# Kernel tuning notes

Measured on AMD Instinct MI355X. Metric: run time of the kernel, lower is better.

The kernel has to match this reference:

```python
import jax, jax.numpy as jnp
import numpy as np

B, S, H = 2, 2048, 2048
NH, NKV, HD = 32, 8, 64
G = NH // NKV  # query heads per KV head
SCALE = HD ** -0.5
NEG = -1e9


def setup_inputs() -> dict:
    key = jax.random.key(0)
    ks = jax.random.split(key, 6)
    hidden_states = jax.random.normal(ks[0], (B, S, H), dtype=jnp.float32)
    # causal additive mask, broadcastable over batch and heads
    causal = jnp.tril(jnp.ones((S, S), dtype=bool))
    attention_mask = jnp.where(causal, 0.0, NEG).astype(jnp.float32)[None, None]
    sd = 1.0 / np.sqrt(H)
    wq = jax.random.normal(ks[1], (H, NH * HD), dtype=jnp.float32) * sd
    wk = jax.random.normal(ks[2], (H, NKV * HD), dtype=jnp.float32) * sd
    wv = jax.random.normal(ks[3], (H, NKV * HD), dtype=jnp.float32) * sd
    wo = jax.random.normal(ks[4], (NH * HD, H), dtype=jnp.float32) * sd
    return {"hidden_states": hidden_states, "attention_mask": attention_mask,
            "wq": wq, "wk": wk, "wv": wv, "wo": wo}


def reference(hidden_states, attention_mask, wq, wk, wv, wo):
    b, s, _ = hidden_states.shape
    # projections; group q heads as [b, kv_head, group, s, d] to avoid
    # materializing expanded K/V (same math as expand+matmul)
    q = (hidden_states @ wq).reshape(b, s, NKV, G, HD)
    k = (hidden_states @ wk).reshape(b, s, NKV, HD)
    v = (hidden_states @ wv).reshape(b, s, NKV, HD)
    q = jnp.einsum('bskgd->bkgsd', q)
    k = jnp.einsum('bskd->bksd', k)
    v = jnp.einsum('bskd->bksd', v)
    scores = jnp.einsum('bkgsd,bktd->bkgst', q, k) * SCALE  # [b,kv,G,s,s]
    mask = attention_mask  # [1,1,S,S] broadcastable
    scores = scores + mask[:, :, None] if mask.ndim == 4 else scores + mask
    attn = jax.nn.softmax(scores.astype(jnp.float32), axis=-1).astype(q.dtype)
    out = jnp.einsum('bkgst,bktd->bkgsd', attn, v)
    out = jnp.einsum('bkgsd->bskgd', out).reshape(b, s, NH * HD)
    return out @ wo
```

## Files before the change

### kernel.cpp

```cpp
#include <hip/hip_runtime.h>
#include <hip/hip_bf16.h>
#include <type_traits>


#define B_SZ 2
#define S_LEN 2048
#define HID 2048
#define NHEADS 32
#define NKVH 8
#define HEADD 64
#define QKV_N 3072
#define QK_SCALE 0.18033688f

typedef __attribute__((ext_vector_type(8))) short bf16x8;
typedef __attribute__((ext_vector_type(4))) float f32x4;

__device__ __forceinline__ float bf2f(unsigned short u) {
  union { unsigned int i; float f; } v;
  v.i = ((unsigned int)u) << 16;
  return v.f;
}
__device__ __forceinline__ unsigned short f2bf(float f) {
  union { float f; unsigned int i; } v;
  v.f = f;
  unsigned int r = v.i + 0x7fffu + ((v.i >> 16) & 1u);
  return (unsigned short)(r >> 16);
}
__device__ __forceinline__ unsigned short f2bf_rn(float f) {
  union { __hip_bfloat16 h; unsigned short u; } cv;
  cv.h = __float2bfloat16(f);
  return cv.u;
}
#if __has_builtin(__builtin_amdgcn_exp2f)
__device__ __forceinline__ float exp2v(float x) { return __builtin_amdgcn_exp2f(x); }
#else
__device__ __forceinline__ float exp2v(float x) { return exp2f(x); }
#endif
__device__ __forceinline__ void gload_lds16(const unsigned short* g, unsigned short* l) {
  __builtin_amdgcn_global_load_lds(
      (const __attribute__((address_space(1))) unsigned int*)g,
      (__attribute__((address_space(3))) unsigned int*)l, 16, 0, 0);
}

__global__ void cvt_bf16_kernel(const float4* __restrict__ in,
                                ushort4* __restrict__ out, int n4) {
  int i = blockIdx.x * blockDim.x + threadIdx.x;
  if (i >= n4) return;
  float4 v = in[i];
  ushort4 o;
  o.x = f2bf(v.x); o.y = f2bf(v.y); o.z = f2bf(v.z); o.w = f2bf(v.w);
  out[i] = o;
}

__global__ void transpose_cvt_kernel(const float* __restrict__ in,
                                     unsigned short* __restrict__ out,
                                     int R, int C, float scale) {
  __shared__ float tile[32][33];
  int c0 = blockIdx.x * 32, r0 = blockIdx.y * 32;
  int x = threadIdx.x, y = threadIdx.y;
#pragma unroll
  for (int i = 0; i < 32; i += 8)
    tile[y + i][x] = in[(size_t)(r0 + y + i) * C + c0 + x];
  __syncthreads();
#pragma unroll
  for (int i = 0; i < 32; i += 8)
    out[(size_t)(c0 + y + i) * R + r0 + x] = f2bf(tile[x][y + i] * scale);
}

__global__ void transpose_v_kernel(const unsigned short* __restrict__ QKV,
                                   unsigned short* __restrict__ Vt) {
  __shared__ unsigned short tile[32][33];
  int s0 = blockIdx.x * 32, d0 = blockIdx.y * 32;
  int bk = blockIdx.z;
  int b = bk >> 3, kvh = bk & 7;
  int x = threadIdx.x, y = threadIdx.y;
#pragma unroll
  for (int i = 0; i < 32; i += 8)
    tile[y + i][x] =
        QKV[(size_t)(b * S_LEN + s0 + y + i) * QKV_N + 2560 + kvh * HEADD + d0 + x];
  __syncthreads();
#pragma unroll
  for (int i = 0; i < 32; i += 8)
    Vt[((size_t)(b * NKVH + kvh) * HEADD + d0 + y + i) * S_LEN + s0 + x] =
        tile[x][y + i];
}

template <typename OutT>
__global__ __launch_bounds__(256) void gemm_bt_kernel(
    const unsigned short* __restrict__ A, const unsigned short* __restrict__ Bt,
    OutT* __restrict__ C, int M, int N, int K) {
  __shared__ unsigned short ldsA[2][128 * 32];
  __shared__ unsigned short ldsB[2][128 * 32];
  const int tid = threadIdx.x;
  const int wave = tid >> 6;
  const int lane = tid & 63;
  const int nwg = gridDim.x;
  const int orig = blockIdx.x;
  const int swz = (orig & 7) * (nwg >> 3) + (orig >> 3);
  const int ntn = N >> 7;
  const int m0 = (swz / ntn) << 7;
  const int n0 = (swz % ntn) << 7;
  const int wr = wave >> 1, wc = wave & 1;
  f32x4 acc[4][4] = {};

  size_t offA[2], offB[2];
#pragma unroll
  for (int i = 0; i < 2; ++i) {
    int cc = tid + i * 256;
    int row = cc >> 2, slot = cc & 3;
    int xk = (slot ^ (row & 3)) * 8;
    offA[i] = (size_t)(m0 + row) * K + xk;
    offB[i] = (size_t)(n0 + row) * K + xk;
  }
  const int rl = lane & 15, g = lane >> 4;
  const int nk = K >> 5;

#pragma unroll
  for (int i = 0; i < 2; ++i) {
    gload_lds16(A + offA[i], &ldsA[0][(wave * 64 + i * 256) * 8]);
    gload_lds16(Bt + offB[i], &ldsB[0][(wave * 64 + i * 256) * 8]);
  }
  __syncthreads();
  int cur = 0;

  for (int t = 0; t < nk; ++t) {
    if (t + 1 < nk) {
      const int k0 = (t + 1) << 5;
      const int nb = cur ^ 1;
#pragma unroll
      for (int i = 0; i < 2; ++i) {
        gload_lds16(A + offA[i] + k0, &ldsA[nb][(wave * 64 + i * 256) * 8]);
        gload_lds16(Bt + offB[i] + k0, &ldsB[nb][(wave * 64 + i * 256) * 8]);
      }
    }
    const int xs = (g ^ (rl & 3)) * 8;
    bf16x8 a[4], b[4];
#pragma unroll
    for (int mi = 0; mi < 4; ++mi)
      a[mi] = *(const bf16x8*)&ldsA[cur][(wr * 64 + mi * 16 + rl) * 32 + xs];
#pragma unroll
    for (int ni = 0; ni < 4; ++ni)
      b[ni] = *(const bf16x8*)&ldsB[cur][(wc * 64 + ni * 16 + rl) * 32 + xs];
#pragma unroll
    for (int mi = 0; mi < 4; ++mi)
#pragma unroll
      for (int ni = 0; ni < 4; ++ni)
        acc[mi][ni] =
            __builtin_amdgcn_mfma_f32_16x16x32_bf16(a[mi], b[ni], acc[mi][ni], 0, 0, 0);
    __syncthreads();
    cur ^= 1;
  }
#pragma unroll
  for (int mi = 0; mi < 4; ++mi)
#pragma unroll
    for (int ni = 0; ni < 4; ++ni)
#pragma unroll
      for (int r = 0; r < 4; ++r) {
        int row = m0 + wr * 64 + mi * 16 + (lane >> 4) * 4 + r;
        int col = n0 + wc * 64 + ni * 16 + (lane & 15);
        float v = acc[mi][ni][r];
        if constexpr (std::is_same_v<OutT, unsigned short>)
          C[(size_t)row * N + col] = f2bf(v);
        else
          C[(size_t)row * N + col] = v;
      }
}

__global__ __launch_bounds__(256) void mfma_attn_kernel(
    const unsigned short* __restrict__ QKV,
    const unsigned short* __restrict__ Vt,
    unsigned short* __restrict__ O) {
  __shared__ unsigned short Ks[2][64 * 64];
  __shared__ unsigned short Vs[2][64 * 64];
  __shared__ unsigned short Pl[4 * 16 * 64];
  const int head = blockIdx.y, b = blockIdx.z;
  const int kvh = head >> 2;
  const int tid = threadIdx.x;
  const int w = tid >> 6, lane = tid & 63;
  const int c = lane & 15, g = lane >> 4;
  unsigned short* Plw = Pl + w * 1024;
  const int srow = tid >> 3, sslot = tid & 7;
  const int xslot = sslot ^ (srow & 7);

  const unsigned short* Ksrc[2];
  const unsigned short* Vsrc[2];
#pragma unroll
  for (int i = 0; i < 2; ++i) {
    int row = srow + i * 32;
    Ksrc[i] = QKV + (size_t)(b * S_LEN + row) * QKV_N + 2048 + kvh * HEADD + xslot * 8;
    Vsrc[i] = Vt + ((size_t)(b * NKVH + kvh) * HEADD + row) * S_LEN + xslot * 8;
  }

#pragma unroll
  for (int i = 0; i < 2; ++i) {
    gload_lds16(Ksrc[i], &Ks[0][(w * 64 + i * 256) * 8]);
    gload_lds16(Vsrc[i], &Vs[0][(w * 64 + i * 256) * 8]);
  }
  __syncthreads();
  int cur = 0;

  for (int ph = 0; ph < 2; ++ph) {
    const int qt = (ph == 0) ? (int)blockIdx.x : (S_LEN / 64 - 1) - (int)blockIdx.x;
    bf16x8 qf[2];
    {
      const unsigned short* qp =
          QKV + (size_t)(b * S_LEN + qt * 64 + w * 16 + c) * QKV_N + head * HEADD +
          g * 8;
      qf[0] = *(const bf16x8*)(qp);
      qf[1] = *(const bf16x8*)(qp + 32);
    }
    f32x4 o_acc[4] = {};
    float mstate = -INFINITY;
    float lstate = 0.f;

    for (int t = 0; t <= qt; ++t) {
      const int kv0 = t * 64;
      const bool has_next = !(ph == 1 && t == qt);
      if (has_next) {
        const int kvn = (t < qt) ? kv0 + 64 : 0;
        const int nb = cur ^ 1;
#pragma unroll
        for (int i = 0; i < 2; ++i) {
          gload_lds16(Ksrc[i] + (size_t)kvn * QKV_N, &Ks[nb][(w * 64 + i * 256) * 8]);
          gload_lds16(Vsrc[i] + kvn, &Vs[nb][(w * 64 + i * 256) * 8]);
        }
      }
      f32x4 s_acc[4] = {};
      __builtin_amdgcn_s_setprio(1);
#pragma unroll
      for (int ks = 0; ks < 2; ++ks)
#pragma unroll
        for (int kn = 0; kn < 4; ++kn) {
          bf16x8 kf = *(const bf16x8*)&Ks[cur][(kn * 16 + c) * 64 +
                                              (((ks * 4 + g) ^ (c & 7)) * 8)];
          s_acc[kn] =
              __builtin_amdgcn_mfma_f32_16x16x32_bf16(kf, qf[ks], s_acc[kn], 0, 0, 0);
        }
      __builtin_amdgcn_s_setprio(0);
      if (t == qt) {
        const int qg = qt * 64 + w * 16 + c;
#pragma unroll
        for (int kn = 0; kn < 4; ++kn)
#pragma unroll
          for (int r = 0; r < 4; ++r)
            if (kv0 + kn * 16 + g * 4 + r > qg) s_acc[kn][r] = -1e30f;
      }
      float mk[4];
#pragma unroll
      for (int kn = 0; kn < 4; ++kn)
        mk[kn] = fmaxf(fmaxf(s_acc[kn][0], s_acc[kn][1]),
                       fmaxf(s_acc[kn][2], s_acc[kn][3]));
      float mx = fmaxf(fmaxf(mk[0], mk[1]), fmaxf(mk[2], mk[3]));
      mx = fmaxf(mx, __shfl_xor(mx, 16));
      mx = fmaxf(mx, __shfl_xor(mx, 32));
      if (__any(mx > mstate + 8.f)) {
        float nm = fmaxf(mstate, mx);
        float al = exp2v(mstate - nm);
        mstate = nm;
        lstate *= al;
        float alr[4];
#pragma unroll
        for (int r = 0; r < 4; ++r) alr[r] = __shfl(al, g * 4 + r);
#pragma unroll
        for (int dn = 0; dn < 4; ++dn)
#pragma unroll
          for (int r = 0; r < 4; ++r) o_acc[dn][r] *= alr[r];
      }
      float rs = 0.f;
#pragma unroll
      for (int kn = 0; kn < 4; ++kn) {
        union { unsigned short u[4]; uint2 v; } pk;
#pragma unroll
        for (int r = 0; r < 4; ++r) {
          float p = exp2v(s_acc[kn][r] - mstate);
          rs += p;
          pk.u[r] = f2bf_rn(p);
        }
        *(uint2*)&Plw[c * 64 + ((kn * 16 + g * 4) ^ ((c & 7) << 3))] = pk.v;
      }
      rs += __shfl_xor(rs, 16);
      rs += __shfl_xor(rs, 32);
      lstate += rs;
      bf16x8 af[2];
#pragma unroll
      for (int ks2 = 0; ks2 < 2; ++ks2)
        af[ks2] = *(const bf16x8*)&Plw[c * 64 + ((ks2 * 32 + g * 8) ^ ((c & 7) << 3))];
      __builtin_amdgcn_s_setprio(1);
#pragma unroll
      for (int ks2 = 0; ks2 < 2; ++ks2)
#pragma unroll
        for (int dn = 0; dn < 4; ++dn) {
          bf16x8 vf = *(const bf16x8*)&Vs[cur][(dn * 16 + c) * 64 +
                                              (((ks2 * 4 + g) ^ (c & 7)) * 8)];
          o_acc[dn] =
              __builtin_amdgcn_mfma_f32_16x16x32_bf16(af[ks2], vf, o_acc[dn], 0, 0, 0);
        }
      __builtin_amdgcn_s_setprio(0);
      __syncthreads();
      if (has_next) cur ^= 1;
    }
    float inv = 1.0f / lstate;
    float invr[4];
#pragma unroll
    for (int r = 0; r < 4; ++r) invr[r] = __shfl(inv, g * 4 + r);
#pragma unroll
    for (int dn = 0; dn < 4; ++dn)
#pragma unroll
      for (int r = 0; r < 4; ++r) {
        int row = qt * 64 + w * 16 + g * 4 + r;
        int col = head * HEADD + dn * 16 + c;
        O[(size_t)(b * S_LEN + row) * (NHEADS * HEADD) + col] =
            f2bf(o_acc[dn][r] * invr[r]);
      }
  }
}

extern "C" void kernel_launch(void* const* d_in, const int* in_sizes, int n_in,
                              void* d_out, int out_size, void* d_ws, size_t ws_size,
                              hipStream_t stream) {
  const float* hs = (const float*)d_in[0];
  const float* wq = (const float*)d_in[2];
  const float* wk = (const float*)d_in[3];
  const float* wv = (const float*)d_in[4];
  const float* wo = (const float*)d_in[5];
  float* out = (float*)d_out;

  char* ws = (char*)d_ws;
  unsigned short* hs_bf = (unsigned short*)(ws);
  unsigned short* wAllT = (unsigned short*)(ws + ((size_t)16 << 20));
  unsigned short* woT  = (unsigned short*)(ws + ((size_t)28 << 20));
  unsigned short* QKV  = (unsigned short*)(ws + ((size_t)36 << 20));
  unsigned short* Ab   = (unsigned short*)(ws + ((size_t)60 << 20));
  unsigned short* VtB  = (unsigned short*)(ws + ((size_t)76 << 20));

  int n4 = (B_SZ * S_LEN * HID) / 4;
  cvt_bf16_kernel<<<n4 / 256, 256, 0, stream>>>((const float4*)hs, (ushort4*)hs_bf, n4);

  dim3 tb(32, 8);
  transpose_cvt_kernel<<<dim3(64, 64), tb, 0, stream>>>(wq, wAllT, HID, 2048, QK_SCALE);
  transpose_cvt_kernel<<<dim3(16, 64), tb, 0, stream>>>(wk, wAllT + (size_t)2048 * HID,
                                                        HID, 512, 1.0f);
  transpose_cvt_kernel<<<dim3(16, 64), tb, 0, stream>>>(wv, wAllT + (size_t)2560 * HID,
                                                        HID, 512, 1.0f);
  transpose_cvt_kernel<<<dim3(64, 64), tb, 0, stream>>>(wo, woT, NHEADS * HEADD, HID,
                                                        1.0f);

  gemm_bt_kernel<unsigned short><<<32 * 24, 256, 0, stream>>>(
      hs_bf, wAllT, QKV, B_SZ * S_LEN, QKV_N, HID);

  transpose_v_kernel<<<dim3(S_LEN / 32, HEADD / 32, B_SZ * NKVH), tb, 0, stream>>>(
      QKV, VtB);

  mfma_attn_kernel<<<dim3(S_LEN / 128, NHEADS, B_SZ), 256, 0, stream>>>(
      QKV, VtB, Ab);

  gemm_bt_kernel<float><<<32 * 16, 256, 0, stream>>>(
      Ab, woT, out, B_SZ * S_LEN, HID, HID);
}
```

Before: 210.6 us.

## Process 128-row query tiles per block with two sub-tiles per wave

Each block now handles one 128-row query tile, with each wave computing two 16-row sub-tiles that share the K/V fragments loaded from LDS. This replaces the earlier scheme of two 64-row tiles processed sequentially per block. It halves K/V streaming per query and reuses LDS reads across sub-tiles, at the cost of losing the balanced front/back pairing of causal work; heavy tiles are scheduled first to compensate. Softmax probabilities are now converted to bf16 by truncation via byte permute instead of round-to-nearest, which is cheaper but slightly less accurate.

```diff
diff --git a/kernel.cpp b/kernel.cpp
--- a/kernel.cpp
+++ b/kernel.cpp
@@ -25,11 +25,6 @@
   v.f = f;
   unsigned int r = v.i + 0x7fffu + ((v.i >> 16) & 1u);
   return (unsigned short)(r >> 16);
-}
-__device__ __forceinline__ unsigned short f2bf_rn(float f) {
-  union { __hip_bfloat16 h; unsigned short u; } cv;
-  cv.h = __float2bfloat16(f);
-  return cv.u;
 }
 #if __has_builtin(__builtin_amdgcn_exp2f)
 __device__ __forceinline__ float exp2v(float x) { return __builtin_amdgcn_exp2f(x); }
@@ -172,13 +167,13 @@
     unsigned short* __restrict__ O) {
   __shared__ unsigned short Ks[2][64 * 64];
   __shared__ unsigned short Vs[2][64 * 64];
-  __shared__ unsigned short Pl[4 * 16 * 64];
+  __shared__ unsigned short Pl[4][2][1024];
   const int head = blockIdx.y, b = blockIdx.z;
   const int kvh = head >> 2;
+  const int qt = 15 - (int)blockIdx.x;
   const int tid = threadIdx.x;
   const int w = tid >> 6, lane = tid & 63;
   const int c = lane & 15, g = lane >> 4;
-  unsigned short* Plw = Pl + w * 1024;
   const int srow = tid >> 3, sslot = tid & 7;
   const int xslot = sslot ^ (srow & 7);
 
@@ -191,6 +186,21 @@
     Vsrc[i] = Vt + ((size_t)(b * NKVH + kvh) * HEADD + row) * S_LEN + xslot * 8;
   }
 
+  const int qg0 = qt * 128 + w * 32;
+  const int qg1 = qg0 + 16;
+  bf16x8 qf0[2], qf1[2];
+  {
+    const unsigned short* qp0 =
+        QKV + (size_t)(b * S_LEN + qg0 + c) * QKV_N + head * HEADD + g * 8;
+    qf0[0] = *(const bf16x8*)(qp0);
+    qf0[1] = *(const bf16x8*)(qp0 + 32);
+    const unsigned short* qp1 = qp0 + (size_t)16 * QKV_N;
+    qf1[0] = *(const bf16x8*)(qp1);
+    qf1[1] = *(const bf16x8*)(qp1 + 32);
+  }
+  f32x4 oa0[4] = {}, oa1[4] = {};
+  float m0s = -INFINITY, l0s = 0.f, m1s = -INFINITY, l1s = 0.f;
+
 #pragma unroll
   for (int i = 0; i < 2; ++i) {
     gload_lds16(Ksrc[i], &Ks[0][(w * 64 + i * 256) * 8]);
@@ -199,107 +209,162 @@
   __syncthreads();
   int cur = 0;
 
-  for (int ph = 0; ph < 2; ++ph) {
-    const int qt = (ph == 0) ? (int)blockIdx.x : (S_LEN / 64 - 1) - (int)blockIdx.x;
-    bf16x8 qf[2];
-    {
-      const unsigned short* qp =
-          QKV + (size_t)(b * S_LEN + qt * 64 + w * 16 + c) * QKV_N + head * HEADD +
-          g * 8;
-      qf[0] = *(const bf16x8*)(qp);
-      qf[1] = *(const bf16x8*)(qp + 32);
-    }
-    f32x4 o_acc[4] = {};
-    float mstate = -INFINITY;
-    float lstate = 0.f;
-
-    for (int t = 0; t <= qt; ++t) {
-      const int kv0 = t * 64;
-      const bool has_next = !(ph == 1 && t == qt);
-      if (has_next) {
-        const int kvn = (t < qt) ? kv0 + 64 : 0;
-        const int nb = cur ^ 1;
-#pragma unroll
-        for (int i = 0; i < 2; ++i) {
-          gload_lds16(Ksrc[i] + (size_t)kvn * QKV_N, &Ks[nb][(w * 64 + i * 256) * 8]);
-          gload_lds16(Vsrc[i] + kvn, &Vs[nb][(w * 64 + i * 256) * 8]);
-        }
-      }
-      f32x4 s_acc[4] = {};
-      __builtin_amdgcn_s_setprio(1);
-#pragma unroll
-      for (int ks = 0; ks < 2; ++ks)
-#pragma unroll
-        for (int kn = 0; kn < 4; ++kn) {
-          bf16x8 kf = *(const bf16x8*)&Ks[cur][(kn * 16 + c) * 64 +
-                                              (((ks * 4 + g) ^ (c & 7)) * 8)];
-          s_acc[kn] =
-              __builtin_amdgcn_mfma_f32_16x16x32_bf16(kf, qf[ks], s_acc[kn], 0, 0, 0);
-        }
-      __builtin_amdgcn_s_setprio(0);
-      if (t == qt) {
-        const int qg = qt * 64 + w * 16 + c;
+  const int tmax = 2 * qt + 1;
+  for (int t = 0; t <= tmax; ++t) {
+    if (t < tmax) {
+      const int kvn = (t + 1) * 64;
+      const int nb = cur ^ 1;
+#pragma unroll
+      for (int i = 0; i < 2; ++i) {
+        gload_lds16(Ksrc[i] + (size_t)kvn * QKV_N, &Ks[nb][(w * 64 + i * 256) * 8]);
+        gload_lds16(Vsrc[i] + kvn, &Vs[nb][(w * 64 + i * 256) * 8]);
+      }
+    }
+    const int kv0 = t * 64;
+    const bool act0 = (kv0 <= qg0 + 15);
+    const bool act1 = (kv0 <= qg1 + 15);
+    f32x4 sa0[4] = {}, sa1[4] = {};
+    __builtin_amdgcn_s_setprio(1);
+#pragma unroll
+    for (int ks = 0; ks < 2; ++ks) {
+      bf16x8 kf[4];
+#pragma unroll
+      for (int kn = 0; kn < 4; ++kn)
+        kf[kn] = *(const bf16x8*)&Ks[cur][(kn * 16 + c) * 64 +
+                                          (((ks * 4 + g) ^ (c & 7)) * 8)];
+      if (act0)
 #pragma unroll
         for (int kn = 0; kn < 4; ++kn)
+          sa0[kn] = __builtin_amdgcn_mfma_f32_16x16x32_bf16(kf[kn], qf0[ks], sa0[kn], 0, 0, 0);
+      if (act1)
+#pragma unroll
+        for (int kn = 0; kn < 4; ++kn)
+          sa1[kn] = __builtin_amdgcn_mfma_f32_16x16x32_bf16(kf[kn], qf1[ks], sa1[kn], 0, 0, 0);
+    }
+    __builtin_amdgcn_s_setprio(0);
+    if (act0) {
+      if (kv0 + 63 > qg0) {
+        const int qrow = qg0 + c;
+#pragma unroll
+        for (int kn = 0; kn < 4; ++kn)
 #pragma unroll
           for (int r = 0; r < 4; ++r)
-            if (kv0 + kn * 16 + g * 4 + r > qg) s_acc[kn][r] = -1e30f;
-      }
-      float mk[4];
-#pragma unroll
-      for (int kn = 0; kn < 4; ++kn)
-        mk[kn] = fmaxf(fmaxf(s_acc[kn][0], s_acc[kn][1]),
-                       fmaxf(s_acc[kn][2], s_acc[kn][3]));
-      float mx = fmaxf(fmaxf(mk[0], mk[1]), fmaxf(mk[2], mk[3]));
+            if (kv0 + kn * 16 + g * 4 + r > qrow) sa0[kn][r] = -1e30f;
+      }
+      float mk0 = fmaxf(fmaxf(sa0[0][0], sa0[0][1]), sa0[0][2]);
+      float mk1 = fmaxf(fmaxf(sa0[0][3], sa0[1][0]), sa0[1][1]);
+      float mk2 = fmaxf(fmaxf(sa0[1][2], sa0[1][3]), sa0[2][0]);
+      float mk3 = fmaxf(fmaxf(sa0[2][1], sa0[2][2]), sa0[2][3]);
+      float mk4 = fmaxf(fmaxf(sa0[3][0], sa0[3][1]), fmaxf(sa0[3][2], sa0[3][3]));
+      float mx = fmaxf(fmaxf(fmaxf(mk0, mk1), fmaxf(mk2, mk3)), mk4);
       mx = fmaxf(mx, __shfl_xor(mx, 16));
       mx = fmaxf(mx, __shfl_xor(mx, 32));
-      if (__any(mx > mstate + 8.f)) {
-        float nm = fmaxf(mstate, mx);
-        float al = exp2v(mstate - nm);
-        mstate = nm;
-        lstate *= al;
+      if (__any(mx > m0s + 8.f)) {
+        float nm = fmaxf(m0s, mx);
+        float al = exp2v(m0s - nm);
+        m0s = nm;
+        l0s *= al;
         float alr[4];
 #pragma unroll
         for (int r = 0; r < 4; ++r) alr[r] = __shfl(al, g * 4 + r);
 #pragma unroll
         for (int dn = 0; dn < 4; ++dn)
 #pragma unroll
-          for (int r = 0; r < 4; ++r) o_acc[dn][r] *= alr[r];
+          for (int r = 0; r < 4; ++r) oa0[dn][r] *= alr[r];
       }
       float rs = 0.f;
 #pragma unroll
       for (int kn = 0; kn < 4; ++kn) {
-        union { unsigned short u[4]; uint2 v; } pk;
-#pragma unroll
-        for (int r = 0; r < 4; ++r) {
-          float p = exp2v(s_acc[kn][r] - mstate);
-          rs += p;
-          pk.u[r] = f2bf_rn(p);
-        }
-        *(uint2*)&Plw[c * 64 + ((kn * 16 + g * 4) ^ ((c & 7) << 3))] = pk.v;
+        float p0 = exp2v(sa0[kn][0] - m0s), p1 = exp2v(sa0[kn][1] - m0s);
+        float p2 = exp2v(sa0[kn][2] - m0s), p3 = exp2v(sa0[kn][3] - m0s);
+        rs += (p0 + p1) + (p2 + p3);
+        uint2 pk;
+        pk.x = __builtin_amdgcn_perm(__float_as_uint(p1), __float_as_uint(p0),
+                                     0x07060302u);
+        pk.y = __builtin_amdgcn_perm(__float_as_uint(p3), __float_as_uint(p2),
+                                     0x07060302u);
+        *(uint2*)&Pl[w][0][c * 64 + ((kn * 16 + g * 4) ^ ((c & 7) << 3))] = pk;
       }
       rs += __shfl_xor(rs, 16);
       rs += __shfl_xor(rs, 32);
-      lstate += rs;
-      bf16x8 af[2];
-#pragma unroll
-      for (int ks2 = 0; ks2 < 2; ++ks2)
-        af[ks2] = *(const bf16x8*)&Plw[c * 64 + ((ks2 * 32 + g * 8) ^ ((c & 7) << 3))];
-      __builtin_amdgcn_s_setprio(1);
-#pragma unroll
-      for (int ks2 = 0; ks2 < 2; ++ks2)
-#pragma unroll
-        for (int dn = 0; dn < 4; ++dn) {
-          bf16x8 vf = *(const bf16x8*)&Vs[cur][(dn * 16 + c) * 64 +
-                                              (((ks2 * 4 + g) ^ (c & 7)) * 8)];
-          o_acc[dn] =
-              __builtin_amdgcn_mfma_f32_16x16x32_bf16(af[ks2], vf, o_acc[dn], 0, 0, 0);
-        }
-      __builtin_amdgcn_s_setprio(0);
-      __syncthreads();
-      if (has_next) cur ^= 1;
-    }
-    float inv = 1.0f / lstate;
+      l0s += rs;
+    }
+    if (act1) {
+      if (kv0 + 63 > qg1) {
+        const int qrow = qg1 + c;
+#pragma unroll
+        for (int kn = 0; kn < 4; ++kn)
+#pragma unroll
+          for (int r = 0; r < 4; ++r)
+            if (kv0 + kn * 16 + g * 4 + r > qrow) sa1[kn][r] = -1e30f;
+      }
+      float mk0 = fmaxf(fmaxf(sa1[0][0], sa1[0][1]), sa1[0][2]);
+      float mk1 = fmaxf(fmaxf(sa1[0][3], sa1[1][0]), sa1[1][1]);
+      float mk2 = fmaxf(fmaxf(sa1[1][2], sa1[1][3]), sa1[2][0]);
+      float mk3 = fmaxf(fmaxf(sa1[2][1], sa1[2][2]), sa1[2][3]);
+      float mk4 = fmaxf(fmaxf(sa1[3][0], sa1[3][1]), fmaxf(sa1[3][2], sa1[3][3]));
+      float mx = fmaxf(fmaxf(fmaxf(mk0, mk1), fmaxf(mk2, mk3)), mk4);
+      mx = fmaxf(mx, __shfl_xor(mx, 16));
+      mx = fmaxf(mx, __shfl_xor(mx, 32));
+      if (__any(mx > m1s + 8.f)) {
+        float nm = fmaxf(m1s, mx);
+        float al = exp2v(m1s - nm);
+        m1s = nm;
+        l1s *= al;
+        float alr[4];
+#pragma unroll
+        for (int r = 0; r < 4; ++r) alr[r] = __shfl(al, g * 4 + r);
+#pragma unroll
+        for (int dn = 0; dn < 4; ++dn)
+#pragma unroll
+          for (int r = 0; r < 4; ++r) oa1[dn][r] *= alr[r];
+      }
+      float rs = 0.f;
+#pragma unroll
+      for (int kn = 0; kn < 4; ++kn) {
+        float p0 = exp2v(sa1[kn][0] - m1s), p1 = exp2v(sa1[kn][1] - m1s);
+        float p2 = exp2v(sa1[kn][2] - m1s), p3 = exp2v(sa1[kn][3] - m1s);
+        rs += (p0 + p1) + (p2 + p3);
+        uint2 pk;
+        pk.x = __builtin_amdgcn_perm(__float_as_uint(p1), __float_as_uint(p0),
+                                     0x07060302u);
+        pk.y = __builtin_amdgcn_perm(__float_as_uint(p3), __float_as_uint(p2),
+                                     0x07060302u);
+        *(uint2*)&Pl[w][1][c * 64 + ((kn * 16 + g * 4) ^ ((c & 7) << 3))] = pk;
+      }
+      rs += __shfl_xor(rs, 16);
+      rs += __shfl_xor(rs, 32);
+      l1s += rs;
+    }
+    __builtin_amdgcn_s_setprio(1);
+#pragma unroll
+    for (int ks2 = 0; ks2 < 2; ++ks2) {
+      bf16x8 vf[4];
+#pragma unroll
+      for (int dn = 0; dn < 4; ++dn)
+        vf[dn] = *(const bf16x8*)&Vs[cur][(dn * 16 + c) * 64 +
+                                          (((ks2 * 4 + g) ^ (c & 7)) * 8)];
+      if (act0) {
+        bf16x8 af = *(const bf16x8*)&Pl[w][0][c * 64 +
+                                              ((ks2 * 32 + g * 8) ^ ((c & 7) << 3))];
+#pragma unroll
+        for (int dn = 0; dn < 4; ++dn)
+          oa0[dn] = __builtin_amdgcn_mfma_f32_16x16x32_bf16(af, vf[dn], oa0[dn], 0, 0, 0);
+      }
+      if (act1) {
+        bf16x8 af = *(const bf16x8*)&Pl[w][1][c * 64 +
+                                              ((ks2 * 32 + g * 8) ^ ((c & 7) << 3))];
+#pragma unroll
+        for (int dn = 0; dn < 4; ++dn)
+          oa1[dn] = __builtin_amdgcn_mfma_f32_16x16x32_bf16(af, vf[dn], oa1[dn], 0, 0, 0);
+      }
+    }
+    __builtin_amdgcn_s_setprio(0);
+    __syncthreads();
+    if (t < tmax) cur ^= 1;
+  }
+  {
+    float inv = 1.0f / l0s;
     float invr[4];
 #pragma unroll
     for (int r = 0; r < 4; ++r) invr[r] = __shfl(inv, g * 4 + r);
@@ -307,10 +372,23 @@
     for (int dn = 0; dn < 4; ++dn)
 #pragma unroll
       for (int r = 0; r < 4; ++r) {
-        int row = qt * 64 + w * 16 + g * 4 + r;
+        int row = qg0 + g * 4 + r;
         int col = head * HEADD + dn * 16 + c;
-        O[(size_t)(b * S_LEN + row) * (NHEADS * HEADD) + col] =
-            f2bf(o_acc[dn][r] * invr[r]);
+        O[(size_t)(b * S_LEN + row) * (NHEADS * HEADD) + col] = f2bf(oa0[dn][r] * invr[r]);
+      }
+  }
+  {
+    float inv = 1.0f / l1s;
+    float invr[4];
+#pragma unroll
+    for (int r = 0; r < 4; ++r) invr[r] = __shfl(inv, g * 4 + r);
+#pragma unroll
+    for (int dn = 0; dn < 4; ++dn)
+#pragma unroll
+      for (int r = 0; r < 4; ++r) {
+        int row = qg1 + g * 4 + r;
+        int col = head * HEADD + dn * 16 + c;
+        O[(size_t)(b * S_LEN + row) * (NHEADS * HEADD) + col] = f2bf(oa1[dn][r] * invr[r]);
       }
   }
 }
@@ -351,8 +429,7 @@
   transpose_v_kernel<<<dim3(S_LEN / 32, HEADD / 32, B_SZ * NKVH), tb, 0, stream>>>(
       QKV, VtB);
 
-  mfma_attn_kernel<<<dim3(S_LEN / 128, NHEADS, B_SZ), 256, 0, stream>>>(
-      QKV, VtB, Ab);
+  mfma_attn_kernel<<<dim3(16, NHEADS, B_SZ), 256, 0, stream>>>(QKV, VtB, Ab);
 
   gemm_bt_kernel<float><<<32 * 16, 256, 0, stream>>>(
       Ab, woT, out, B_SZ * S_LEN, HID, HID);
```

Result: slower. 303.5 us (+44.1%).
